# Kernel optimization log

Measured on AMD Instinct MI355X. Metric: run time of the kernel, lower is better.

The kernel has to match this reference:

```python
import jax, jax.numpy as jnp
import numpy as np
from jax import lax

DWT_SCALE = 0.5
IDWT_SCALE = 1.0
PAD = 2  # (kernel_size-1)//2 for k=5


def haar_dwt(x, s):
    """x: [B,C,H,W] -> (ll, lh, hl, hh) each [B,C,H/2,W/2]. 2x2 Haar, scale s."""
    a = x[..., 0::2, 0::2]
    b = x[..., 0::2, 1::2]
    c = x[..., 1::2, 0::2]
    d = x[..., 1::2, 1::2]
    ll = s * (a + b + c + d)
    lh = s * (a + b - c - d)
    hl = s * (a - b + c - d)
    hh = s * (a - b - c + d)
    return ll, lh, hl, hh


def haar_idwt(ll, lh, hl, hh, s):
    """Inverse of haar_dwt when s_dwt * s_idwt_total = 0.5. Returns [B,C,2H,2W]."""
    a = s * (ll + lh + hl + hh)
    b = s * (ll + lh - hl - hh)
    c = s * (ll - lh + hl - hh)
    d = s * (ll - lh - hl + hh)
    B, C, H2, W2 = ll.shape
    top = jnp.stack([a, b], axis=-1).reshape(B, C, H2, 2 * W2)  # even rows
    bot = jnp.stack([c, d], axis=-1).reshape(B, C, H2, 2 * W2)  # odd rows
    return jnp.stack([top, bot], axis=-2).reshape(B, C, 2 * H2, 2 * W2)


def conv2d(x, w, pad):
    return lax.conv_general_dilated(
        x, w, window_strides=(1, 1), padding=[(pad, pad), (pad, pad)],
        dimension_numbers=("NCHW", "OIHW", "NCHW"))


def setup_inputs() -> dict:
    key = jax.random.key(0)
    kx, k0, k1, k2, kb = jax.random.split(key, 5)
    C, K = 64, 5
    x = jax.random.normal(kx, (8, C, 256, 256), dtype=jnp.float32)
    # kaiming_uniform-ish small init to keep 3-level recursion numerically tame
    scale = 0.02
    w0 = jax.random.normal(k0, (4 * C, 4 * C, K, K), dtype=jnp.float32) * scale
    w1 = jax.random.normal(k1, (4 * C, 4 * C, K, K), dtype=jnp.float32) * scale
    w2 = jax.random.normal(k2, (4 * C, 4 * C, K, K), dtype=jnp.float32) * scale
    bias = jax.random.normal(kb, (C,), dtype=jnp.float32) * 0.01
    return {"x": x, "w0": w0, "w1": w1, "w2": w2, "bias": bias}


def reference(x, w0, w1, w2, bias):
    weights = [w0, w1, w2]
    idwt_s = DWT_SCALE * IDWT_SCALE  # perfect reconstruction pair
    curr = x
    ll_levels, high_levels = [], []
    for w in weights:
        ll, lh, hl, hh = haar_dwt(curr, DWT_SCALE)
        curr = ll  # pre-conv LL feeds the next level
        B, C, H2, W2 = ll.shape
        stacked = jnp.stack([ll, lh, hl, hh], axis=2).reshape(B, 4 * C, H2, W2)
        y = conv2d(stacked, w, PAD)  # [B, 4*Co, H2, W2]
        y = y.reshape(B, -1, 4, H2, W2)
        ll_levels.append(y[:, :, 0])
        high_levels.append(y[:, :, 1:])
    next_ll = jnp.zeros_like(ll_levels[-1])
    for ll_t, h_t in zip(reversed(ll_levels), reversed(high_levels)):
        ll = ll_t + next_ll
        next_ll = haar_idwt(ll, h_t[:, :, 0], h_t[:, :, 1], h_t[:, :, 2], idwt_s)
    return next_ll + bias.reshape(1, -1, 1, 1)
```

## Files before the change

kernel.cpp:

```cpp
#include <hip/hip_runtime.h>


typedef unsigned short u16;
typedef __attribute__((ext_vector_type(8))) __bf16 bf16x8;
typedef __attribute__((ext_vector_type(4))) float f32x4;

__device__ __forceinline__ u16 f2bf(float f) {
  union { float f; unsigned u; } v; v.f = f;
  unsigned r = v.u + 0x7fffu + ((v.u >> 16) & 1u);
  return (u16)(r >> 16);
}
__device__ __forceinline__ float bf2f(u16 u) {
  union { unsigned u; float f; } v; v.u = ((unsigned)u) << 16;
  return v.f;
}

typedef const unsigned int __attribute__((address_space(1)))* gas1_t;
typedef unsigned int __attribute__((address_space(3)))* gas3_t;
__device__ __forceinline__ void gload16(const void* g, void* l) {
  __builtin_amdgcn_global_load_lds((gas1_t)g, (gas3_t)l, 16, 0, 0);
}

__global__ void k_wtrans3(const float* __restrict__ wa, const float* __restrict__ wb_,
                          const float* __restrict__ wc, u16* __restrict__ oa,
                          u16* __restrict__ ob, u16* __restrict__ oc) {
  const float* w = (blockIdx.y == 0) ? wa : (blockIdx.y == 1) ? wb_ : wc;
  u16* o = (blockIdx.y == 0) ? oa : (blockIdx.y == 1) ? ob : oc;
  int co = blockIdx.x;
  int ci = threadIdx.x;
  const float* src = w + ((long)co * 256 + ci) * 25;
  float v[25];
#pragma unroll
  for (int tp = 0; tp < 25; ++tp) v[tp] = src[tp];
#pragma unroll
  for (int tp = 0; tp < 25; ++tp)
    o[((long)tp * 256 + co) * 256 + ci] = f2bf(v[tp]);
}

__global__ void k_border(u16* __restrict__ st, int B_, int H2, int W2) {
  int PW = W2 + 4;
  int npix = 4 * PW + 4 * H2;
  int gid = blockIdx.x * blockDim.x + threadIdx.x;
  int pid = gid >> 6, lane = gid & 63;
  if (pid >= B_ * npix) return;
  int b = pid / npix, p = pid % npix;
  int row, col;
  if (p < 2 * PW) { row = p / PW; col = p % PW; }
  else if (p < 4 * PW) { int q = p - 2 * PW; row = H2 + 2 + q / PW; col = q % PW; }
  else { int q = p - 4 * PW; row = 2 + (q >> 2); int c4 = q & 3; col = (c4 < 2) ? c4 : W2 + c4; }
  long base = (((long)b * (H2 + 4) + row) * PW + col) * 256 + lane * 4;
  *(ushort4*)(st + base) = make_ushort4(0, 0, 0, 0);
}

__global__ void k_dwt(const float* __restrict__ in, u16* __restrict__ st,
                      float* __restrict__ ll, int B_, int H2, int W2) {
  int idx = blockIdx.x * blockDim.x + threadIdx.x;
  int W2h = W2 >> 1;
  int total = B_ * 64 * H2 * W2h;
  if (idx >= total) return;
  int w2h = idx % W2h; int t2 = idx / W2h;
  int h2 = t2 % H2; t2 /= H2;
  int c = t2 % 64; int b = t2 / 64;
  int w2 = w2h * 2;
  const float* r0 = in + (((long)(b * 64 + c) * (2 * H2) + 2 * h2) * (2 * W2)) + 2 * w2;
  const float* r1 = r0 + 2 * W2;
  float4 tp = *(const float4*)r0;
  float4 bt = *(const float4*)r1;
  float ll0 = 0.5f * (tp.x + tp.y + bt.x + bt.y);
  float lh0 = 0.5f * (tp.x + tp.y - bt.x - bt.y);
  float hl0 = 0.5f * (tp.x - tp.y + bt.x - bt.y);
  float hh0 = 0.5f * (tp.x - tp.y - bt.x + bt.y);
  float ll1 = 0.5f * (tp.z + tp.w + bt.z + bt.w);
  float lh1 = 0.5f * (tp.z + tp.w - bt.z - bt.w);
  float hl1 = 0.5f * (tp.z - tp.w + bt.z - bt.w);
  float hh1 = 0.5f * (tp.z - tp.w - bt.z + bt.w);
  long sbase = (((long)b * (H2 + 4) + (h2 + 2)) * (W2 + 4) + (w2 + 2)) * 256 + 4 * c;
  *(ushort4*)(st + sbase)       = make_ushort4(f2bf(ll0), f2bf(lh0), f2bf(hl0), f2bf(hh0));
  *(ushort4*)(st + sbase + 256) = make_ushort4(f2bf(ll1), f2bf(lh1), f2bf(hl1), f2bf(hh1));
  long lbase = (((long)(b * 64 + c) * H2) + h2) * W2 + w2;
  *(float2*)(ll + lbase) = make_float2(ll0, ll1);
}

__global__ __launch_bounds__(512, 2) void k_conv8(
    const u16* __restrict__ st, const u16* __restrict__ wt, u16* __restrict__ out,
    int H2, int W2, int ktot, int nsplit) {
  __shared__ __align__(16) char smem[131072];
  const int t = threadIdx.x;
  const int lane = t & 63;
  const int wv = t >> 6;
  const int wm = wv >> 2, wn = wv & 3;
  const int nwg = gridDim.x;
  const int bid = blockIdx.x;
  const int lb = (bid & 7) * (nwg >> 3) + (bid >> 3);
  const int m0 = lb * 256;
  const int PW = W2 + 4;
  const int spl = blockIdx.y;
  const int kk0 = (spl * ktot) / nsplit;
  const int kk1 = ((spl + 1) * ktot) / nsplit;
  const long Mrows = (long)nwg * 256;
  u16* yo = out + (long)spl * Mrows * 256;

  const int trow = t >> 3;
  const int srcci = ((t & 7) ^ (trow & 7)) * 8;
  const char* baseA[4];
#pragma unroll
  for (int u = 0; u < 4; ++u) {
    int m = m0 + u * 64 + trow;
    int w = m % W2; int q = m / W2;
    int hh = q % H2; int b = q / H2;
    long sp = ((long)(b * (H2 + 4) + hh + 2) * PW + (w + 2));
    baseA[u] = (const char*)(st + sp * 256 + srcci);
  }
  const char* baseB0 = (const char*)(wt + trow * 256 + srcci);

  f32x4 acc[8][4];
#pragma unroll
  for (int i = 0; i < 8; ++i)
#pragma unroll
    for (int j = 0; j < 4; ++j) acc[i][j] = f32x4{0.f, 0.f, 0.f, 0.f};

  const int kq = (lane >> 4) * 16;
  const int sw = (lane & 7) << 4;
  int va0 = (wm * 128 + (lane & 15)) * 128 + (kq ^ sw);
  int va1 = (wm * 128 + (lane & 15)) * 128 + ((64 + kq) ^ sw);
  int vb0 = 32768 + (wn * 64 + (lane & 15)) * 128 + (kq ^ sw);
  int vb1 = 32768 + (wn * 64 + (lane & 15)) * 128 + ((64 + kq) ^ sw);

  bf16x8 a0[4][2], a1[4][2], b0[2][2], b1[2][2];

  auto offsets = [&](int kk, long& oA, long& oB) {
    int tap = kk >> 2, cic = kk & 3;
    int dy = tap / 5 - 2, dx = tap % 5 - 2;
    oA = ((long)(dy * PW + dx) * 256 + cic * 64) * 2;
    oB = ((long)tap * 65536 + cic * 64) * 2;
  };
  auto stageA4 = [&](long off, int dsto) {
    char* d = smem + dsto + wv * 1024;
#pragma unroll
    for (int u = 0; u < 4; ++u) gload16(baseA[u] + off, d + u * 8192);
  };
  auto stageB4 = [&](long off, int dsto) {
    char* d = smem + dsto + 32768 + wv * 1024;
#pragma unroll
    for (int u = 0; u < 4; ++u) gload16(baseB0 + u * 32768 + off, d + u * 8192);
  };

#define LDA0 { _Pragma("unroll") for (int i = 0; i < 4; ++i) {       \
    a0[i][0] = *(const bf16x8*)(smem + va0 + i * 2048);              \
    a0[i][1] = *(const bf16x8*)(smem + va1 + i * 2048); } }
#define LDA1 { _Pragma("unroll") for (int i = 0; i < 4; ++i) {       \
    a1[i][0] = *(const bf16x8*)(smem + va0 + 8192 + i * 2048);       \
    a1[i][1] = *(const bf16x8*)(smem + va1 + 8192 + i * 2048); } }
#define LDB0 { _Pragma("unroll") for (int j = 0; j < 2; ++j) {       \
    b0[j][0] = *(const bf16x8*)(smem + vb0 + j * 2048);              \
    b0[j][1] = *(const bf16x8*)(smem + vb1 + j * 2048); } }
#define LDB1 { _Pragma("unroll") for (int j = 0; j < 2; ++j) {       \
    b1[j][0] = *(const bf16x8*)(smem + vb0 + 4096 + j * 2048);       \
    b1[j][1] = *(const bf16x8*)(smem + vb1 + 4096 + j * 2048); } }
#define MMQ(A, B, IB, JB)                                                     \
  _Pragma("unroll") for (int i = 0; i < 4; ++i)                               \
  _Pragma("unroll") for (int j = 0; j < 2; ++j)                               \
  _Pragma("unroll") for (int k = 0; k < 2; ++k)                               \
    acc[(IB) + i][(JB) + j] = __builtin_amdgcn_mfma_f32_16x16x32_bf16(        \
        A[i][k], B[j][k], acc[(IB) + i][(JB) + j], 0, 0, 0);

  long oA, oB;
  offsets(kk0, oA, oB);
  stageA4(oA, 0); stageB4(oB, 0);
  offsets(kk0 + 1, oA, oB);
  stageA4(oA, 65536); stageB4(oB, 65536);
  asm volatile("s_waitcnt vmcnt(8)" ::: "memory");
  __builtin_amdgcn_s_barrier();
  LDA0 LDB0

  int curo = 0;
  for (int kt = kk0; kt < kk1; ++kt) {
    const bool stg = (kt + 2) < kk1;
    const bool rd1 = (kt + 1) < kk1;
    LDA1 LDB1
    va0 ^= 65536; va1 ^= 65536; vb0 ^= 65536; vb1 ^= 65536;
    __builtin_amdgcn_s_barrier();
    asm volatile("s_waitcnt lgkmcnt(12)" ::: "memory");
    __builtin_amdgcn_sched_barrier(0);
    __builtin_amdgcn_s_setprio(1);
    MMQ(a0, b0, 0, 0)
    __builtin_amdgcn_s_setprio(0);
    __builtin_amdgcn_s_barrier();
    asm volatile("s_waitcnt lgkmcnt(4)" ::: "memory");
    __builtin_amdgcn_sched_barrier(0);
    __builtin_amdgcn_s_setprio(1);
    MMQ(a1, b0, 4, 0)
    __builtin_amdgcn_s_setprio(0);
    if (rd1) { asm volatile("s_waitcnt vmcnt(0)" ::: "memory"); }
    __builtin_amdgcn_s_barrier();
    asm volatile("s_waitcnt lgkmcnt(0)" ::: "memory");
    __builtin_amdgcn_sched_barrier(0);
    __builtin_amdgcn_s_setprio(1);
    MMQ(a1, b1, 4, 2)
    __builtin_amdgcn_s_setprio(0);
    if (rd1) { LDB0 }
    if (stg) { offsets(kt + 2, oA, oB); stageA4(oA, curo); }
    __builtin_amdgcn_s_barrier();
    __builtin_amdgcn_s_setprio(1);
    MMQ(a0, b1, 0, 2)
    __builtin_amdgcn_s_setprio(0);
    if (stg) { stageB4(oB, curo); }
    if (rd1) { LDA0 }
    curo ^= 65536;
  }
#undef MMQ
#undef LDA0
#undef LDA1
#undef LDB0
#undef LDB1

#pragma unroll
  for (int i = 0; i < 8; ++i) {
    int mloc = m0 + wm * 128 + i * 16 + (lane >> 4) * 4;
#pragma unroll
    for (int j = 0; j < 4; ++j) {
      int nloc = wn * 64 + j * 16 + (lane & 15);
#pragma unroll
      for (int r = 0; r < 4; ++r)
        yo[(long)(mloc + r) * 256 + nloc] = f2bf(acc[i][j][r]);
    }
  }
}

__global__ void k_idwt(const u16* __restrict__ P, long psz, int ns,
                       const float* __restrict__ nll, const float* __restrict__ bias,
                       float* __restrict__ out, int B_, int H2, int W2) {
  int idx = blockIdx.x * blockDim.x + threadIdx.x;
  int W2h = W2 >> 1;
  int total = B_ * 64 * H2 * W2h;
  if (idx >= total) return;
  int w2h = idx % W2h; int t2 = idx / W2h;
  int h2 = t2 % H2; t2 /= H2;
  int c = t2 % 64; int b = t2 / 64;
  int w2 = w2h * 2;
  long ybase = (((long)b * H2 + h2) * W2 + w2) * 256 + 4 * c;
  float s[8] = {0.f, 0.f, 0.f, 0.f, 0.f, 0.f, 0.f, 0.f};
  for (int k = 0; k < ns; ++k) {
    const u16* p = P + (long)k * psz + ybase;
    ushort4 q0 = *(const ushort4*)(p);
    ushort4 q1 = *(const ushort4*)(p + 256);
    s[0] += bf2f(q0.x); s[1] += bf2f(q0.y); s[2] += bf2f(q0.z); s[3] += bf2f(q0.w);
    s[4] += bf2f(q1.x); s[5] += bf2f(q1.y); s[6] += bf2f(q1.z); s[7] += bf2f(q1.w);
  }
  float llv0 = s[0], lh0 = s[1], hl0 = s[2], hh0 = s[3];
  float llv1 = s[4], lh1 = s[5], hl1 = s[6], hh1 = s[7];
  if (nll) {
    float2 nv = *(const float2*)(nll + (((long)(b * 64 + c) * H2 + h2) * W2 + w2));
    llv0 += nv.x; llv1 += nv.y;
  }
  float bv = bias ? bias[c] : 0.f;
  float a0 = 0.5f * (llv0 + lh0 + hl0 + hh0) + bv;
  float b0 = 0.5f * (llv0 + lh0 - hl0 - hh0) + bv;
  float c0 = 0.5f * (llv0 - lh0 + hl0 - hh0) + bv;
  float d0 = 0.5f * (llv0 - lh0 - hl0 + hh0) + bv;
  float a1 = 0.5f * (llv1 + lh1 + hl1 + hh1) + bv;
  float b1 = 0.5f * (llv1 + lh1 - hl1 - hh1) + bv;
  float c1 = 0.5f * (llv1 - lh1 + hl1 - hh1) + bv;
  float d1 = 0.5f * (llv1 - lh1 - hl1 + hh1) + bv;
  long obase = (((long)(b * 64 + c) * (2 * H2) + 2 * h2) * (2 * W2)) + 2 * w2;
  *(float4*)(out + obase)          = make_float4(a0, b0, a1, b1);
  *(float4*)(out + obase + 2 * W2) = make_float4(c0, d0, c1, d1);
}

constexpr size_t WBF_SZ1 = 25ull * 256 * 256 * 2;
constexpr size_t OFF_WBF = 0;
constexpr size_t OFF_S0  = 3 * WBF_SZ1;
constexpr size_t S0_SZ   = 8ull * 132 * 132 * 256 * 2;
constexpr size_t OFF_L0  = OFF_S0 + S0_SZ;
constexpr size_t OFF_Y0  = OFF_L0 + 8ull * 64 * 128 * 128 * 4;
constexpr size_t REL_S1 = 0;
constexpr size_t REL_L1 = 8ull * 68 * 68 * 256 * 2;
constexpr size_t REL_S2 = REL_L1 + 8ull * 64 * 64 * 64 * 4;
constexpr size_t REL_P2 = REL_S2 + 8ull * 36 * 36 * 256 * 2;
constexpr size_t REL_N2 = 0;
constexpr size_t REL_N1 = 8ull * 64 * 64 * 64 * 4;
constexpr size_t REL_L2 = 0;

extern "C" void kernel_launch(void* const* d_in, const int* in_sizes, int n_in,
                              void* d_out, int out_size, void* d_ws, size_t ws_size,
                              hipStream_t stream) {
  const float* x    = (const float*)d_in[0];
  const float* w0   = (const float*)d_in[1];
  const float* w1   = (const float*)d_in[2];
  const float* w2   = (const float*)d_in[3];
  const float* bias = (const float*)d_in[4];
  float* out = (float*)d_out;
  char* ws = (char*)d_ws;

  u16* wbf0 = (u16*)(ws + OFF_WBF);
  u16* wbf1 = (u16*)(ws + OFF_WBF + WBF_SZ1);
  u16* wbf2 = (u16*)(ws + OFF_WBF + 2 * WBF_SZ1);
  u16* s0   = (u16*)(ws + OFF_S0);
  u16* s1   = (u16*)(ws + OFF_S0 + REL_S1);
  float* l1 = (float*)(ws + OFF_S0 + REL_L1);
  u16* s2   = (u16*)(ws + OFF_S0 + REL_S2);
  u16* P2   = (u16*)(ws + OFF_S0 + REL_P2);
  float* n2 = (float*)(ws + OFF_S0 + REL_N2);
  float* n1 = (float*)(ws + OFF_S0 + REL_N1);
  float* l2 = (float*)(ws + OFF_S0 + REL_L2);
  float* l0 = (float*)(ws + OFF_L0);
  u16* P1   = (u16*)(ws + OFF_L0);
  u16* y0   = (u16*)(ws + OFF_Y0);

  k_wtrans3<<<dim3(256, 3), 256, 0, stream>>>(w0, w1, w2, wbf0, wbf1, wbf2);

  k_border<<<2080, 256, 0, stream>>>(s0, 8, 128, 128);
  k_dwt<<<16384, 256, 0, stream>>>(x, s0, l0, 8, 128, 128);
  k_conv8<<<dim3(512, 1), 512, 0, stream>>>(s0, wbf0, y0, 128, 128, 100, 1);

  k_border<<<1056, 256, 0, stream>>>(s1, 8, 64, 64);
  k_border<<<544, 256, 0, stream>>>(s2, 8, 32, 32);

  k_dwt<<<4096, 256, 0, stream>>>(l0, s1, l1, 8, 64, 64);
  k_conv8<<<dim3(128, 2), 512, 0, stream>>>(s1, wbf1, P1, 64, 64, 100, 2);

  k_dwt<<<1024, 256, 0, stream>>>(l1, s2, l2, 8, 32, 32);
  k_conv8<<<dim3(32, 8), 512, 0, stream>>>(s2, wbf2, P2, 32, 32, 100, 8);

  k_idwt<<<1024, 256, 0, stream>>>(P2, 2097152L, 8, nullptr, nullptr, n2, 8, 32, 32);
  k_idwt<<<4096, 256, 0, stream>>>(P1, 8388608L, 2, n2, nullptr, n1, 8, 64, 64);
  k_idwt<<<16384, 256, 0, stream>>>(y0, 33554432L, 1, n1, bias, out, 8, 128, 128);
}
```

Measured before the change: 636.6 us.

## Restructure conv GEMM to 1024-thread blocks with 32-channel K tiles

Rewrites the implicit-GEMM convolution kernel to use 16 waves per block, each computing a 64x64 output tile, with a K step of 32 channels, so there are twice as many K iterations. Shared memory per block drops to 64 KB, and each thread issues one A load and one B load per stage. The aim is higher occupancy and simpler per-iteration scheduling. In exchange it drops the XOR swizzle on the LDS layout, which risks bank conflicts. It also doubles the barrier count per unit of work and halves per-wave MFMA reuse. The launch bounds request an occupancy the hardware may not be able to provide, which can force the compiler into register pressure.

```diff
diff --git a/kernel.cpp b/kernel.cpp
--- a/kernel.cpp
+++ b/kernel.cpp
@@ -81,10 +81,10 @@
   *(float2*)(ll + lbase) = make_float2(ll0, ll1);
 }
 
-__global__ __launch_bounds__(512, 2) void k_conv8(
+__global__ __launch_bounds__(1024, 4) void k_conv32(
     const u16* __restrict__ st, const u16* __restrict__ wt, u16* __restrict__ out,
     int H2, int W2, int ktot, int nsplit) {
-  __shared__ __align__(16) char smem[131072];
+  __shared__ __align__(16) char smem[65536];
   const int t = threadIdx.x;
   const int lane = t & 63;
   const int wv = t >> 6;
@@ -97,126 +97,91 @@
   const int spl = blockIdx.y;
   const int kk0 = (spl * ktot) / nsplit;
   const int kk1 = ((spl + 1) * ktot) / nsplit;
-  const long Mrows = (long)nwg * 256;
-  u16* yo = out + (long)spl * Mrows * 256;
-
-  const int trow = t >> 3;
-  const int srcci = ((t & 7) ^ (trow & 7)) * 8;
-  const char* baseA[4];
-#pragma unroll
-  for (int u = 0; u < 4; ++u) {
-    int m = m0 + u * 64 + trow;
+  u16* yo = out + (long)spl * ((long)nwg * 256) * 256;
+
+  const char* baseA;
+  {
+    int m = m0 + (t >> 2);
     int w = m % W2; int q = m / W2;
     int hh = q % H2; int b = q / H2;
     long sp = ((long)(b * (H2 + 4) + hh + 2) * PW + (w + 2));
-    baseA[u] = (const char*)(st + sp * 256 + srcci);
-  }
-  const char* baseB0 = (const char*)(wt + trow * 256 + srcci);
-
-  f32x4 acc[8][4];
-#pragma unroll
-  for (int i = 0; i < 8; ++i)
+    baseA = (const char*)(st + sp * 256 + (t & 3) * 8);
+  }
+  const char* baseB = (const char*)(wt + (t >> 2) * 256 + (t & 3) * 8);
+
+  f32x4 acc[4][4];
+#pragma unroll
+  for (int i = 0; i < 4; ++i)
 #pragma unroll
     for (int j = 0; j < 4; ++j) acc[i][j] = f32x4{0.f, 0.f, 0.f, 0.f};
 
-  const int kq = (lane >> 4) * 16;
-  const int sw = (lane & 7) << 4;
-  int va0 = (wm * 128 + (lane & 15)) * 128 + (kq ^ sw);
-  int va1 = (wm * 128 + (lane & 15)) * 128 + ((64 + kq) ^ sw);
-  int vb0 = 32768 + (wn * 64 + (lane & 15)) * 128 + (kq ^ sw);
-  int vb1 = 32768 + (wn * 64 + (lane & 15)) * 128 + ((64 + kq) ^ sw);
-
-  bf16x8 a0[4][2], a1[4][2], b0[2][2], b1[2][2];
+  int va = (wm * 64 + (lane & 15)) * 64 + ((lane >> 4) << 4);
+  int vb = 16384 + (wn * 64 + (lane & 15)) * 64 + ((lane >> 4) << 4);
+
+  bf16x8 a01[2], a23[2], bb[4];
 
   auto offsets = [&](int kk, long& oA, long& oB) {
-    int tap = kk >> 2, cic = kk & 3;
+    int tap = kk >> 3, cic = kk & 7;
     int dy = tap / 5 - 2, dx = tap % 5 - 2;
-    oA = ((long)(dy * PW + dx) * 256 + cic * 64) * 2;
-    oB = ((long)tap * 65536 + cic * 64) * 2;
+    oA = ((long)(dy * PW + dx) * 256 + cic * 32) * 2;
+    oB = ((long)tap * 65536 + cic * 32) * 2;
   };
-  auto stageA4 = [&](long off, int dsto) {
-    char* d = smem + dsto + wv * 1024;
-#pragma unroll
-    for (int u = 0; u < 4; ++u) gload16(baseA[u] + off, d + u * 8192);
+  auto stage2 = [&](long oA, long oB, int dsto) {
+    gload16(baseA + oA, smem + dsto + wv * 1024);
+    gload16(baseB + oB, smem + dsto + 16384 + wv * 1024);
   };
-  auto stageB4 = [&](long off, int dsto) {
-    char* d = smem + dsto + 32768 + wv * 1024;
-#pragma unroll
-    for (int u = 0; u < 4; ++u) gload16(baseB0 + u * 32768 + off, d + u * 8192);
-  };
-
-#define LDA0 { _Pragma("unroll") for (int i = 0; i < 4; ++i) {       \
-    a0[i][0] = *(const bf16x8*)(smem + va0 + i * 2048);              \
-    a0[i][1] = *(const bf16x8*)(smem + va1 + i * 2048); } }
-#define LDA1 { _Pragma("unroll") for (int i = 0; i < 4; ++i) {       \
-    a1[i][0] = *(const bf16x8*)(smem + va0 + 8192 + i * 2048);       \
-    a1[i][1] = *(const bf16x8*)(smem + va1 + 8192 + i * 2048); } }
-#define LDB0 { _Pragma("unroll") for (int j = 0; j < 2; ++j) {       \
-    b0[j][0] = *(const bf16x8*)(smem + vb0 + j * 2048);              \
-    b0[j][1] = *(const bf16x8*)(smem + vb1 + j * 2048); } }
-#define LDB1 { _Pragma("unroll") for (int j = 0; j < 2; ++j) {       \
-    b1[j][0] = *(const bf16x8*)(smem + vb0 + 4096 + j * 2048);       \
-    b1[j][1] = *(const bf16x8*)(smem + vb1 + 4096 + j * 2048); } }
-#define MMQ(A, B, IB, JB)                                                     \
-  _Pragma("unroll") for (int i = 0; i < 4; ++i)                               \
-  _Pragma("unroll") for (int j = 0; j < 2; ++j)                               \
-  _Pragma("unroll") for (int k = 0; k < 2; ++k)                               \
-    acc[(IB) + i][(JB) + j] = __builtin_amdgcn_mfma_f32_16x16x32_bf16(        \
-        A[i][k], B[j][k], acc[(IB) + i][(JB) + j], 0, 0, 0);
+
+#define LDEND { a01[0] = *(const bf16x8*)(smem + va);                 \
+    a01[1] = *(const bf16x8*)(smem + va + 1024);                      \
+    _Pragma("unroll") for (int j = 0; j < 4; ++j)                     \
+      bb[j] = *(const bf16x8*)(smem + vb + j * 1024); }
+#define MM2(A2, I0)                                                   \
+  _Pragma("unroll") for (int i2 = 0; i2 < 2; ++i2)                    \
+  _Pragma("unroll") for (int j = 0; j < 4; ++j)                       \
+    acc[(I0) + i2][j] = __builtin_amdgcn_mfma_f32_16x16x32_bf16(      \
+        A2[i2], bb[j], acc[(I0) + i2][j], 0, 0, 0);
 
   long oA, oB;
   offsets(kk0, oA, oB);
-  stageA4(oA, 0); stageB4(oB, 0);
+  stage2(oA, oB, 0);
   offsets(kk0 + 1, oA, oB);
-  stageA4(oA, 65536); stageB4(oB, 65536);
-  asm volatile("s_waitcnt vmcnt(8)" ::: "memory");
+  stage2(oA, oB, 32768);
+  asm volatile("s_waitcnt vmcnt(2)" ::: "memory");
   __builtin_amdgcn_s_barrier();
-  LDA0 LDB0
+  LDEND
 
   int curo = 0;
   for (int kt = kk0; kt < kk1; ++kt) {
     const bool stg = (kt + 2) < kk1;
     const bool rd1 = (kt + 1) < kk1;
-    LDA1 LDB1
-    va0 ^= 65536; va1 ^= 65536; vb0 ^= 65536; vb1 ^= 65536;
+    a23[0] = *(const bf16x8*)(smem + va + 2048);
+    a23[1] = *(const bf16x8*)(smem + va + 3072);
+    va ^= 32768; vb ^= 32768;
     __builtin_amdgcn_s_barrier();
-    asm volatile("s_waitcnt lgkmcnt(12)" ::: "memory");
+    asm volatile("s_waitcnt lgkmcnt(2)" ::: "memory");
     __builtin_amdgcn_sched_barrier(0);
     __builtin_amdgcn_s_setprio(1);
-    MMQ(a0, b0, 0, 0)
-    __builtin_amdgcn_s_setprio(0);
-    __builtin_amdgcn_s_barrier();
-    asm volatile("s_waitcnt lgkmcnt(4)" ::: "memory");
-    __builtin_amdgcn_sched_barrier(0);
-    __builtin_amdgcn_s_setprio(1);
-    MMQ(a1, b0, 4, 0)
+    MM2(a01, 0)
     __builtin_amdgcn_s_setprio(0);
     if (rd1) { asm volatile("s_waitcnt vmcnt(0)" ::: "memory"); }
     __builtin_amdgcn_s_barrier();
     asm volatile("s_waitcnt lgkmcnt(0)" ::: "memory");
     __builtin_amdgcn_sched_barrier(0);
     __builtin_amdgcn_s_setprio(1);
-    MMQ(a1, b1, 4, 2)
+    MM2(a23, 2)
     __builtin_amdgcn_s_setprio(0);
-    if (rd1) { LDB0 }
-    if (stg) { offsets(kt + 2, oA, oB); stageA4(oA, curo); }
-    __builtin_amdgcn_s_barrier();
-    __builtin_amdgcn_s_setprio(1);
-    MMQ(a0, b1, 0, 2)
-    __builtin_amdgcn_s_setprio(0);
-    if (stg) { stageB4(oB, curo); }
-    if (rd1) { LDA0 }
-    curo ^= 65536;
-  }
-#undef MMQ
-#undef LDA0
-#undef LDA1
-#undef LDB0
-#undef LDB1
-
-#pragma unroll
-  for (int i = 0; i < 8; ++i) {
-    int mloc = m0 + wm * 128 + i * 16 + (lane >> 4) * 4;
+    __builtin_amdgcn_sched_barrier(0);
+    if (stg) { offsets(kt + 2, oA, oB); stage2(oA, oB, curo); }
+    if (rd1) { LDEND }
+    __builtin_amdgcn_sched_barrier(0);
+    curo ^= 32768;
+  }
+#undef MM2
+#undef LDEND
+
+#pragma unroll
+  for (int i = 0; i < 4; ++i) {
+    int mloc = m0 + wm * 64 + i * 16 + (lane >> 4) * 4;
 #pragma unroll
     for (int j = 0; j < 4; ++j) {
       int nloc = wn * 64 + j * 16 + (lane & 15);
@@ -311,16 +276,16 @@
 
   k_border<<<2080, 256, 0, stream>>>(s0, 8, 128, 128);
   k_dwt<<<16384, 256, 0, stream>>>(x, s0, l0, 8, 128, 128);
-  k_conv8<<<dim3(512, 1), 512, 0, stream>>>(s0, wbf0, y0, 128, 128, 100, 1);
+  k_conv32<<<dim3(512, 1), 1024, 0, stream>>>(s0, wbf0, y0, 128, 128, 200, 1);
 
   k_border<<<1056, 256, 0, stream>>>(s1, 8, 64, 64);
   k_border<<<544, 256, 0, stream>>>(s2, 8, 32, 32);
 
   k_dwt<<<4096, 256, 0, stream>>>(l0, s1, l1, 8, 64, 64);
-  k_conv8<<<dim3(128, 2), 512, 0, stream>>>(s1, wbf1, P1, 64, 64, 100, 2);
+  k_conv32<<<dim3(128, 2), 1024, 0, stream>>>(s1, wbf1, P1, 64, 64, 200, 2);
 
   k_dwt<<<1024, 256, 0, stream>>>(l1, s2, l2, 8, 32, 32);
-  k_conv8<<<dim3(32, 8), 512, 0, stream>>>(s2, wbf2, P2, 32, 32, 100, 8);
+  k_conv32<<<dim3(32, 8), 1024, 0, stream>>>(s2, wbf2, P2, 32, 32, 200, 8);
 
   k_idwt<<<1024, 256, 0, stream>>>(P2, 2097152L, 8, nullptr, nullptr, n2, 8, 32, 32);
   k_idwt<<<4096, 256, 0, stream>>>(P1, 8388608L, 2, n2, nullptr, n1, 8, 64, 64);
```

Result: slower. 713.5 us (+12.1%).

## Halve conv K-tile to 32 channels, shrinking LDS to 64KB per block

Applied to the files above, without the earlier changes.

The implicit-GEMM conv kernel now stages 32 input channels per K-step instead of 64. The shared-memory double buffer drops from 128KB to 64KB, and each block does twice as many K iterations (200 instead of 100). The LDS swizzle, fragment loads, wait counts and the staging layout are reworked to match. The aim is to cut LDS footprint so blocks are less limited by shared memory. The cost is twice as many barriers and pipeline steps per unit of MFMA work, with less compute to hide load latency in each step.

```diff
diff --git a/kernel.cpp b/kernel.cpp
--- a/kernel.cpp
+++ b/kernel.cpp
@@ -81,10 +81,10 @@
   *(float2*)(ll + lbase) = make_float2(ll0, ll1);
 }
 
-__global__ __launch_bounds__(512, 2) void k_conv8(
+__global__ __launch_bounds__(512, 2) void k_conv32(
     const u16* __restrict__ st, const u16* __restrict__ wt, u16* __restrict__ out,
     int H2, int W2, int ktot, int nsplit) {
-  __shared__ __align__(16) char smem[131072];
+  __shared__ __align__(16) char smem[65536];
   const int t = threadIdx.x;
   const int lane = t & 63;
   const int wv = t >> 6;
@@ -97,21 +97,19 @@
   const int spl = blockIdx.y;
   const int kk0 = (spl * ktot) / nsplit;
   const int kk1 = ((spl + 1) * ktot) / nsplit;
-  const long Mrows = (long)nwg * 256;
-  u16* yo = out + (long)spl * Mrows * 256;
-
-  const int trow = t >> 3;
-  const int srcci = ((t & 7) ^ (trow & 7)) * 8;
-  const char* baseA[4];
-#pragma unroll
-  for (int u = 0; u < 4; ++u) {
-    int m = m0 + u * 64 + trow;
+  u16* yo = out + (long)spl * ((long)nwg * 256) * 256;
+
+  const int srcsl = ((t & 3) ^ ((t >> 3) & 3)) * 8;
+  const char* baseA[2];
+#pragma unroll
+  for (int u = 0; u < 2; ++u) {
+    int m = m0 + u * 128 + (t >> 2);
     int w = m % W2; int q = m / W2;
     int hh = q % H2; int b = q / H2;
     long sp = ((long)(b * (H2 + 4) + hh + 2) * PW + (w + 2));
-    baseA[u] = (const char*)(st + sp * 256 + srcci);
-  }
-  const char* baseB0 = (const char*)(wt + trow * 256 + srcci);
+    baseA[u] = (const char*)(st + sp * 256 + srcsl);
+  }
+  const char* baseB = (const char*)(wt + (t >> 2) * 256 + srcsl);
 
   f32x4 acc[8][4];
 #pragma unroll
@@ -119,57 +117,49 @@
 #pragma unroll
     for (int j = 0; j < 4; ++j) acc[i][j] = f32x4{0.f, 0.f, 0.f, 0.f};
 
-  const int kq = (lane >> 4) * 16;
-  const int sw = (lane & 7) << 4;
-  int va0 = (wm * 128 + (lane & 15)) * 128 + (kq ^ sw);
-  int va1 = (wm * 128 + (lane & 15)) * 128 + ((64 + kq) ^ sw);
-  int vb0 = 32768 + (wn * 64 + (lane & 15)) * 128 + (kq ^ sw);
-  int vb1 = 32768 + (wn * 64 + (lane & 15)) * 128 + ((64 + kq) ^ sw);
-
-  bf16x8 a0[4][2], a1[4][2], b0[2][2], b1[2][2];
+  const int swz = ((lane & 15) >> 1) & 3;
+  int va = (wm * 128 + (lane & 15)) * 64 + (((lane >> 4) ^ swz) << 4);
+  int vb = 16384 + (wn * 64 + (lane & 15)) * 64 + (((lane >> 4) ^ swz) << 4);
+
+  bf16x8 a0[4], a1[4], b0[2], b1[2];
 
   auto offsets = [&](int kk, long& oA, long& oB) {
-    int tap = kk >> 2, cic = kk & 3;
+    int tap = kk >> 3, cic = kk & 7;
     int dy = tap / 5 - 2, dx = tap % 5 - 2;
-    oA = ((long)(dy * PW + dx) * 256 + cic * 64) * 2;
-    oB = ((long)tap * 65536 + cic * 64) * 2;
+    oA = ((long)(dy * PW + dx) * 256 + cic * 32) * 2;
+    oB = ((long)tap * 65536 + cic * 32) * 2;
   };
-  auto stageA4 = [&](long off, int dsto) {
-    char* d = smem + dsto + wv * 1024;
-#pragma unroll
-    for (int u = 0; u < 4; ++u) gload16(baseA[u] + off, d + u * 8192);
+  auto stageA = [&](long oA, int dsto) {
+#pragma unroll
+    for (int u = 0; u < 2; ++u)
+      gload16(baseA[u] + oA, smem + dsto + u * 8192 + wv * 1024);
   };
-  auto stageB4 = [&](long off, int dsto) {
-    char* d = smem + dsto + 32768 + wv * 1024;
-#pragma unroll
-    for (int u = 0; u < 4; ++u) gload16(baseB0 + u * 32768 + off, d + u * 8192);
+  auto stageB = [&](long oB, int dsto) {
+#pragma unroll
+    for (int u = 0; u < 2; ++u)
+      gload16(baseB + u * 65536 + oB, smem + dsto + 16384 + u * 8192 + wv * 1024);
   };
 
-#define LDA0 { _Pragma("unroll") for (int i = 0; i < 4; ++i) {       \
-    a0[i][0] = *(const bf16x8*)(smem + va0 + i * 2048);              \
-    a0[i][1] = *(const bf16x8*)(smem + va1 + i * 2048); } }
-#define LDA1 { _Pragma("unroll") for (int i = 0; i < 4; ++i) {       \
-    a1[i][0] = *(const bf16x8*)(smem + va0 + 8192 + i * 2048);       \
-    a1[i][1] = *(const bf16x8*)(smem + va1 + 8192 + i * 2048); } }
-#define LDB0 { _Pragma("unroll") for (int j = 0; j < 2; ++j) {       \
-    b0[j][0] = *(const bf16x8*)(smem + vb0 + j * 2048);              \
-    b0[j][1] = *(const bf16x8*)(smem + vb1 + j * 2048); } }
-#define LDB1 { _Pragma("unroll") for (int j = 0; j < 2; ++j) {       \
-    b1[j][0] = *(const bf16x8*)(smem + vb0 + 4096 + j * 2048);       \
-    b1[j][1] = *(const bf16x8*)(smem + vb1 + 4096 + j * 2048); } }
+#define LDA0 { _Pragma("unroll") for (int i = 0; i < 4; ++i)          \
+    a0[i] = *(const bf16x8*)(smem + va + i * 1024); }
+#define LDA1 { _Pragma("unroll") for (int i = 0; i < 4; ++i)          \
+    a1[i] = *(const bf16x8*)(smem + va + 4096 + i * 1024); }
+#define LDB0 { _Pragma("unroll") for (int j = 0; j < 2; ++j)          \
+    b0[j] = *(const bf16x8*)(smem + vb + j * 1024); }
+#define LDB1 { _Pragma("unroll") for (int j = 0; j < 2; ++j)          \
+    b1[j] = *(const bf16x8*)(smem + vb + 2048 + j * 1024); }
 #define MMQ(A, B, IB, JB)                                                     \
   _Pragma("unroll") for (int i = 0; i < 4; ++i)                               \
   _Pragma("unroll") for (int j = 0; j < 2; ++j)                               \
-  _Pragma("unroll") for (int k = 0; k < 2; ++k)                               \
     acc[(IB) + i][(JB) + j] = __builtin_amdgcn_mfma_f32_16x16x32_bf16(        \
-        A[i][k], B[j][k], acc[(IB) + i][(JB) + j], 0, 0, 0);
+        A[i], B[j], acc[(IB) + i][(JB) + j], 0, 0, 0);
 
   long oA, oB;
   offsets(kk0, oA, oB);
-  stageA4(oA, 0); stageB4(oB, 0);
+  stageA(oA, 0); stageB(oB, 0);
   offsets(kk0 + 1, oA, oB);
-  stageA4(oA, 65536); stageB4(oB, 65536);
-  asm volatile("s_waitcnt vmcnt(8)" ::: "memory");
+  stageA(oA, 32768); stageB(oB, 32768);
+  asm volatile("s_waitcnt vmcnt(4)" ::: "memory");
   __builtin_amdgcn_s_barrier();
   LDA0 LDB0
 
@@ -178,15 +168,15 @@
     const bool stg = (kt + 2) < kk1;
     const bool rd1 = (kt + 1) < kk1;
     LDA1 LDB1
-    va0 ^= 65536; va1 ^= 65536; vb0 ^= 65536; vb1 ^= 65536;
+    va ^= 32768; vb ^= 32768;
     __builtin_amdgcn_s_barrier();
-    asm volatile("s_waitcnt lgkmcnt(12)" ::: "memory");
+    asm volatile("s_waitcnt lgkmcnt(6)" ::: "memory");
     __builtin_amdgcn_sched_barrier(0);
     __builtin_amdgcn_s_setprio(1);
     MMQ(a0, b0, 0, 0)
     __builtin_amdgcn_s_setprio(0);
     __builtin_amdgcn_s_barrier();
-    asm volatile("s_waitcnt lgkmcnt(4)" ::: "memory");
+    asm volatile("s_waitcnt lgkmcnt(2)" ::: "memory");
     __builtin_amdgcn_sched_barrier(0);
     __builtin_amdgcn_s_setprio(1);
     MMQ(a1, b0, 4, 0)
@@ -199,14 +189,14 @@
     MMQ(a1, b1, 4, 2)
     __builtin_amdgcn_s_setprio(0);
     if (rd1) { LDB0 }
-    if (stg) { offsets(kt + 2, oA, oB); stageA4(oA, curo); }
+    if (stg) { offsets(kt + 2, oA, oB); stageA(oA, curo); }
     __builtin_amdgcn_s_barrier();
     __builtin_amdgcn_s_setprio(1);
     MMQ(a0, b1, 0, 2)
     __builtin_amdgcn_s_setprio(0);
-    if (stg) { stageB4(oB, curo); }
+    if (stg) { stageB(oB, curo); }
     if (rd1) { LDA0 }
-    curo ^= 65536;
+    curo ^= 32768;
   }
 #undef MMQ
 #undef LDA0
@@ -311,16 +301,16 @@
 
   k_border<<<2080, 256, 0, stream>>>(s0, 8, 128, 128);
   k_dwt<<<16384, 256, 0, stream>>>(x, s0, l0, 8, 128, 128);
-  k_conv8<<<dim3(512, 1), 512, 0, stream>>>(s0, wbf0, y0, 128, 128, 100, 1);
+  k_conv32<<<dim3(512, 1), 512, 0, stream>>>(s0, wbf0, y0, 128, 128, 200, 1);
 
   k_border<<<1056, 256, 0, stream>>>(s1, 8, 64, 64);
   k_border<<<544, 256, 0, stream>>>(s2, 8, 32, 32);
 
   k_dwt<<<4096, 256, 0, stream>>>(l0, s1, l1, 8, 64, 64);
-  k_conv8<<<dim3(128, 2), 512, 0, stream>>>(s1, wbf1, P1, 64, 64, 100, 2);
+  k_conv32<<<dim3(128, 2), 512, 0, stream>>>(s1, wbf1, P1, 64, 64, 200, 2);
 
   k_dwt<<<1024, 256, 0, stream>>>(l1, s2, l2, 8, 32, 32);
-  k_conv8<<<dim3(32, 8), 512, 0, stream>>>(s2, wbf2, P2, 32, 32, 100, 8);
+  k_conv32<<<dim3(32, 8), 512, 0, stream>>>(s2, wbf2, P2, 32, 32, 200, 8);
 
   k_idwt<<<1024, 256, 0, stream>>>(P2, 2097152L, 8, nullptr, nullptr, n2, 8, 32, 32);
   k_idwt<<<4096, 256, 0, stream>>>(P1, 8388608L, 2, n2, nullptr, n1, 8, 64, 64);
```

Result: slower. 687.3 us (+8.0%).
